# Performance work log

Hardware: AMD Instinct MI355X
Metric: run time of the kernel (lower is better)

## Reference

```python
import jax, jax.numpy as jnp
import numpy as np

COMMITMENT_COST = 0.25


def setup_inputs() -> dict:
    key = jax.random.key(0)
    k1, k2 = jax.random.split(key)
    # z_latents: [B, H, W, D] encoder output latents
    z_latents = jax.random.normal(k1, (128, 32, 32, 64), dtype=jnp.float32)
    # embeddings: [D, K] codebook, uniform init like tf.random_uniform_initializer (default [-0.05, 0.05])
    embeddings = jax.random.uniform(k2, (64, 1024), dtype=jnp.float32, minval=-0.05, maxval=0.05)
    return {"z_latents": z_latents, "embeddings": embeddings}


def reference(z_latents, embeddings):
    d, k = embeddings.shape
    flat = z_latents.reshape(-1, d)  # [N, D]
    # squared L2 distances to each codebook entry: [N, K]
    distances = (
        jnp.sum(flat * flat, axis=1, keepdims=True)
        - 2.0 * (flat @ embeddings)
        + jnp.sum(embeddings * embeddings, axis=0, keepdims=True)
    )
    # argmax(-d) == argmin(d) (both take first occurrence on ties)
    encoding_indices = jnp.argmin(distances, axis=1)  # [N]
    # one-hot @ embeddings.T is just a gather of codebook rows
    quantized = jnp.take(embeddings.T, encoding_indices, axis=0).reshape(z_latents.shape)
    commitment_loss = jnp.mean((jax.lax.stop_gradient(quantized) - z_latents) ** 2)
    embedding_loss = jnp.mean((jax.lax.stop_gradient(z_latents) - quantized) ** 2)
    vq_loss = embedding_loss + COMMITMENT_COST * commitment_loss
    # straight-through estimator
    quantized_st = z_latents + jax.lax.stop_gradient(quantized - z_latents)
    return quantized_st, vq_loss
```

## Files before the change

### kernel.cpp

```cpp
#include <hip/hip_runtime.h>

#pragma clang fp contract(off)

typedef __attribute__((ext_vector_type(8))) short short8;
typedef __attribute__((ext_vector_type(4))) float f32x4;

#define MARGIN 0.02f

static __device__ __forceinline__ unsigned short f2b(float f) {
    union { float f; unsigned u; } x; x.f = f;
    unsigned u = x.u;
    return (unsigned short)((u + 0x7FFFu + ((u >> 16) & 1u)) >> 16);
}

template <int ES>
static __device__ __forceinline__ float np_dist(
    const float* __restrict__ zr, const float* __restrict__ ecol,
    float zn, float en) {
    float c = 0.f;
    #pragma unroll
    for (int i = 0; i < 64; ++i) c = fmaf(zr[i], ecol[i * ES], c);
    float t = zn - 2.f * c;
    return t + en;
}

template <bool ET>
__global__ __launch_bounds__(256) void vq_prep(
    const float* __restrict__ E, float* __restrict__ enorm,
    float* __restrict__ Et, unsigned* __restrict__ EbW) {
    __shared__ float sT[64][65];
    const int tid = threadIdx.x;
    const int w = tid >> 6;
    const int m64 = tid & 63;
    const int c0 = blockIdx.x * 64;

    #pragma unroll
    for (int r = 0; r < 16; ++r) {
        const int row = r * 4 + w;
        sT[row][m64] = E[row * 1024 + c0 + m64];
    }
    __syncthreads();

    if (ET) {
        #pragma unroll
        for (int it = 0; it < 16; ++it) {
            const int e = it * 256 + tid;
            const int col = e >> 6, d = e & 63;
            Et[(c0 + col) * 64 + d] = sT[d][col];
        }
    }
    #pragma unroll
    for (int it = 0; it < 8; ++it) {
        const int w0 = it * 256 + tid;
        const int cl = w0 >> 9;
        const int s = (w0 >> 8) & 1;
        const int ll = (w0 >> 2) & 63;
        const int j = (w0 & 3) * 2;
        const int d = s * 32 + (ll >> 4) * 8 + j;
        const int col = cl * 16 + (ll & 15);
        const unsigned lo = f2b(sT[d][col]);
        const unsigned hi = f2b(sT[d + 1][col]);
        EbW[(blockIdx.x * 4 + cl) * 512 + (w0 & 511)] = lo | (hi << 16);
    }
    if (tid < 64) {
        float s2 = 0.f;
        #pragma unroll
        for (int d = 0; d < 64; ++d) {
            float v = sT[d][tid];
            s2 = fmaf(v, v, s2);
        }
        enorm[c0 + tid] = s2;
    }
}

template <int MODE>
__global__ __launch_bounds__(256, 8) void vq_main(
    const float* __restrict__ z, const float* __restrict__ E,
    const float* __restrict__ Et, const unsigned short* __restrict__ Eb,
    const float* __restrict__ enorm, float* __restrict__ out) {
    __shared__ unsigned short sB[2][4096];
    __shared__ float sEn[1024];

    float* sZn = (float*)&sB[0][0];
    int* sIdx = (int*)((char*)&sB[0][0] + 256);
    float* sRed = (float*)((char*)&sB[0][0] + 512);

    const int tid = threadIdx.x;
    const int w = tid >> 6;
    const int l = tid & 63;
    const int quad = l >> 4;
    const int m = l & 15;
    const int b = blockIdx.x;

    auto stage = [&](int h, int buf) {
        const unsigned short* gp = Eb + h * 4096 + w * 1024 + l * 8;
        unsigned short* lp = &sB[buf][w * 1024];
        #pragma unroll
        for (int i = 0; i < 2; ++i) {
            __builtin_amdgcn_global_load_lds(
                (const __attribute__((address_space(1))) void*)(gp + i * 512),
                (__attribute__((address_space(3))) void*)(lp + i * 512),
                16, 0, 0);
        }
    };

    if constexpr (MODE < 2) {
        stage(0, 0);
        stage(1, 1);
        float4 e4 = ((const float4*)enorm)[tid];
        e4.x *= 0.5f; e4.y *= 0.5f; e4.z *= 0.5f; e4.w *= 0.5f;
        ((float4*)sEn)[tid] = e4;
    } else {
        #pragma unroll
        for (int i = 0; i < 4; ++i) {
            const int col = tid + i * 256;
            float s2 = 0.f;
            #pragma unroll
            for (int d = 0; d < 64; ++d) {
                float v = E[d * 1024 + col];
                s2 = fmaf(v, v, s2);
            }
            sEn[col] = s2 * 0.5f;
        }
    }

    short8 a[2];
    {
        const int rowl = w * 16 + m;
        #pragma unroll
        for (int s = 0; s < 2; ++s) {
            const float* zp = z + (b * 64 + rowl) * 64 + s * 32 + quad * 8;
            union { float4 v; float f[4]; } u0, u1;
            u0.v = *(const float4*)zp;
            u1.v = *(const float4*)(zp + 4);
            short8 av;
            #pragma unroll
            for (int j = 0; j < 4; ++j) av[j] = (short)(f2b(u0.f[j]) ^ 0x8000u);
            #pragma unroll
            for (int j = 0; j < 4; ++j) av[4 + j] = (short)(f2b(u1.f[j]) ^ 0x8000u);
            a[s] = av;
        }
    }

    float v1p[4], v2p[4];
    #pragma unroll
    for (int r = 0; r < 4; ++r) { v1p[r] = 3.4e38f; v2p[r] = 3.4e38f; }

    if constexpr (MODE < 2) {
        asm volatile("s_waitcnt vmcnt(2) lgkmcnt(0)" ::: "memory");
        __builtin_amdgcn_sched_barrier(0);
        __builtin_amdgcn_s_barrier();

        for (int h = 0; h < 16; ++h) {
            const unsigned short* bufp = &sB[h & 1][l * 8];
            #pragma unroll
            for (int ct = 0; ct < 4; ++ct) {
                const int c = h * 4 + ct;
                short8 b0 = *(const short8*)(bufp + ct * 1024);
                short8 b1 = *(const short8*)(bufp + ct * 1024 + 512);
                const float enh = sEn[c * 16 + m];
                f32x4 acc = {enh, enh, enh, enh};
                acc = __builtin_amdgcn_mfma_f32_16x16x32_bf16(a[0], b0, acc, 0, 0, 0);
                acc = __builtin_amdgcn_mfma_f32_16x16x32_bf16(a[1], b1, acc, 0, 0, 0);
                #pragma unroll
                for (int r = 0; r < 4; ++r) {
                    float p0 = __uint_as_float(
                        (__float_as_uint(acc[r]) & 0xFFFFFFC0u) | (unsigned)c);
                    v2p[r] = __builtin_amdgcn_fmed3f(p0, v1p[r], v2p[r]);
                    v1p[r] = fminf(p0, v1p[r]);
                }
            }
            if (h == 15) break;
            __builtin_amdgcn_s_barrier();
            if (h < 14) {
                stage(h + 2, h & 1);
                asm volatile("s_waitcnt vmcnt(2)" ::: "memory");
            } else {
                asm volatile("s_waitcnt vmcnt(0)" ::: "memory");
            }
            __builtin_amdgcn_sched_barrier(0);
            __builtin_amdgcn_s_barrier();
        }
    } else {
        unsigned* sW = (unsigned*)&sB[0][0];
        __syncthreads();
        for (int h = 0; h < 16; ++h) {
            #pragma unroll
            for (int it = 0; it < 8; ++it) {
                const int w0 = it * 256 + tid;
                const int cl = w0 >> 9;
                const int s = (w0 >> 8) & 1;
                const int ll = (w0 >> 2) & 63;
                const int j = (w0 & 3) * 2;
                const int d = s * 32 + (ll >> 4) * 8 + j;
                const int col = (h * 4 + cl) * 16 + (ll & 15);
                const unsigned lo = f2b(E[d * 1024 + col]);
                const unsigned hi = f2b(E[(d + 1) * 1024 + col]);
                sW[w0] = lo | (hi << 16);
            }
            __syncthreads();
            const unsigned short* bufp = &sB[0][l * 8];
            #pragma unroll
            for (int ct = 0; ct < 4; ++ct) {
                const int c = h * 4 + ct;
                short8 b0 = *(const short8*)(bufp + ct * 1024);
                short8 b1 = *(const short8*)(bufp + ct * 1024 + 512);
                const float enh = sEn[c * 16 + m];
                f32x4 acc = {enh, enh, enh, enh};
                acc = __builtin_amdgcn_mfma_f32_16x16x32_bf16(a[0], b0, acc, 0, 0, 0);
                acc = __builtin_amdgcn_mfma_f32_16x16x32_bf16(a[1], b1, acc, 0, 0, 0);
                #pragma unroll
                for (int r = 0; r < 4; ++r) {
                    float p0 = __uint_as_float(
                        (__float_as_uint(acc[r]) & 0xFFFFFFC0u) | (unsigned)c);
                    v2p[r] = __builtin_amdgcn_fmed3f(p0, v1p[r], v2p[r]);
                    v1p[r] = fminf(p0, v1p[r]);
                }
            }
            __syncthreads();
        }
    }

    __syncthreads();

    if (l < 16) {
        const int row = w * 16 + l;
        const float* zr = z + (b * 64 + row) * 64;
        float S[16];
        #pragma unroll
        for (int u = 0; u < 16; ++u) { float v = zr[u]; S[u] = v * v; }
        #pragma unroll
        for (int t = 1; t < 4; ++t)
            #pragma unroll
            for (int u = 0; u < 16; ++u) {
                float v = zr[16 * t + u];
                float sq = v * v;
                S[u] = S[u] + sq;
            }
        float R0 = (S[0] + S[4]) + (S[8] + S[12]);
        float R1 = (S[1] + S[5]) + (S[9] + S[13]);
        float R2 = (S[2] + S[6]) + (S[10] + S[14]);
        float R3 = (S[3] + S[7]) + (S[11] + S[15]);
        sZn[row] = (R0 + R1) + (R2 + R3);
    }
    __syncthreads();

    constexpr bool viaEt = (MODE == 0);
    const float margin_q = MARGIN * 0.5f;
    float la = 0.f;
    #pragma unroll
    for (int r = 0; r < 4; ++r) {
        float pv1 = v1p[r];
        float vb = pv1;
        #pragma unroll
        for (int mask = 1; mask <= 8; mask <<= 1)
            vb = fminf(vb, __shfl_xor(vb, mask));
        const int rowl = w * 16 + quad * 4 + r;
        const float zn = sZn[rowl];
        const float* zr = z + (b * 64 + rowl) * 64;
        float d = 3.4e38f;
        int kk = 0x7fffffff;
        if (pv1 <= vb + margin_q) {
            kk = (int)(__float_as_uint(pv1) & 63u) * 16 + m;
            d = viaEt ? np_dist<1>(zr, Et + kk * 64, zn, 2.f * sEn[kk])
                      : np_dist<1024>(zr, E + kk, zn, 2.f * sEn[kk]);
        }
        float pv2 = v2p[r];
        if (pv2 <= vb + margin_q) {
            int kc = (int)(__float_as_uint(pv2) & 63u) * 16 + m;
            float dd = viaEt ? np_dist<1>(zr, Et + kc * 64, zn, 2.f * sEn[kc])
                             : np_dist<1024>(zr, E + kc, zn, 2.f * sEn[kc]);
            if (dd < d || (dd == d && kc < kk)) { d = dd; kk = kc; }
        }
        #pragma unroll
        for (int mask = 1; mask <= 8; mask <<= 1) {
            float d2 = __shfl_xor(d, mask);
            int c2 = __shfl_xor(kk, mask);
            bool take = (d2 < d) || (d2 == d && c2 < kk);
            d = take ? d2 : d;
            kk = take ? c2 : kk;
        }
        if (m == 0) {
            sIdx[rowl] = kk;
            la += d;
        }
    }
    __syncthreads();

    {
        const int row_local = w * 16 + (l >> 2);
        const int part = l & 3;
        const int idx = sIdx[row_local];
        union { float s[16]; float4 f[4]; } tmp;
        if (viaEt) {
            const float4* src = (const float4*)(Et + idx * 64 + part * 16);
            #pragma unroll
            for (int q4 = 0; q4 < 4; ++q4) tmp.f[q4] = src[q4];
        } else {
            #pragma unroll
            for (int dd = 0; dd < 16; ++dd) tmp.s[dd] = E[(part * 16 + dd) * 1024 + idx];
        }
        float4* dst = (float4*)(out + (b * 64 + row_local) * 64 + part * 16);
        #pragma unroll
        for (int q4 = 0; q4 < 4; ++q4) dst[q4] = tmp.f[q4];
    }

    #pragma unroll
    for (int mask = 32; mask >= 1; mask >>= 1) la += __shfl_xor(la, mask);
    if (l == 0) sRed[w] = la;
    __syncthreads();

    if (tid == 0) {
        const float blocksum = sRed[0] + sRed[1] + sRed[2] + sRed[3];
        atomicAdd(out + 8388608, blocksum * (1.25f / 8388608.f));
    }
}

extern "C" void kernel_launch(void* const* d_in, const int* in_sizes, int n_in,
                              void* d_out, int out_size, void* d_ws, size_t ws_size,
                              hipStream_t stream) {
    const float* z = (const float*)d_in[0];
    const float* E = (const float*)d_in[1];
    float* out = (float*)d_out;

    char* ws = (char*)d_ws;
    float* enorm = (float*)(ws + 128);
    unsigned short* Eb = (unsigned short*)(ws + 8192);
    float* Et = (float*)(ws + 139264);

    if (ws_size >= (size_t)401408) {
        vq_prep<true><<<16, 256, 0, stream>>>(E, enorm, Et, (unsigned*)Eb);
        vq_main<0><<<2048, 256, 0, stream>>>(z, E, Et, Eb, enorm, out);
    } else if (ws_size >= (size_t)139264) {
        vq_prep<false><<<16, 256, 0, stream>>>(E, enorm, Et, (unsigned*)Eb);
        vq_main<1><<<2048, 256, 0, stream>>>(z, E, Et, Eb, enorm, out);
    } else {
        vq_main<2><<<2048, 256, 0, stream>>>(z, E, Et, Eb, enorm, out);
    }
}
```

Baseline: 145.2 us.

## Use 512-thread blocks with 32 rows per wave and half-codebook LDS staging

Blocks now hold 8 waves, and each wave covers 32 rows as two 16-row MFMA tiles, so every B fragment read from LDS feeds two MFMA tiles. The bf16 codebook is staged in two halves of 64KB each rather than a double-buffered 4-chunk ring, which cuts the number of barriers from 30 to a few. Row norms are now computed before the main loop and shared with a shuffle instead of through LDS, and the indices are kept per wave, which removes several block syncs. The cost is much larger LDS per block (about 68KB), which lowers occupancy. Loads of the second half are also not overlapped with compute, so the wait is exposed.

```diff
diff --git a/kernel.cpp b/kernel.cpp
--- a/kernel.cpp
+++ b/kernel.cpp
@@ -74,16 +74,14 @@
 }
 
 template <int MODE>
-__global__ __launch_bounds__(256, 8) void vq_main(
+__global__ __launch_bounds__(512, 4) void vq_main(
     const float* __restrict__ z, const float* __restrict__ E,
     const float* __restrict__ Et, const unsigned short* __restrict__ Eb,
     const float* __restrict__ enorm, float* __restrict__ out) {
-    __shared__ unsigned short sB[2][4096];
+    __shared__ unsigned short sB[32768];
     __shared__ float sEn[1024];
-
-    float* sZn = (float*)&sB[0][0];
-    int* sIdx = (int*)((char*)&sB[0][0] + 256);
-    float* sRed = (float*)((char*)&sB[0][0] + 512);
+    __shared__ int sIdxW[8][32];
+    __shared__ float sRed[8];
 
     const int tid = threadIdx.x;
     const int w = tid >> 6;
@@ -91,12 +89,13 @@
     const int quad = l >> 4;
     const int m = l & 15;
     const int b = blockIdx.x;
-
-    auto stage = [&](int h, int buf) {
-        const unsigned short* gp = Eb + h * 4096 + w * 1024 + l * 8;
-        unsigned short* lp = &sB[buf][w * 1024];
-        #pragma unroll
-        for (int i = 0; i < 2; ++i) {
+    const int R0 = (b * 8 + w) * 32;
+
+    auto stageH = [&](int H) {
+        const unsigned short* gp = Eb + H * 32768 + w * 4096 + l * 8;
+        unsigned short* lp = &sB[w * 4096];
+        #pragma unroll
+        for (int i = 0; i < 8; ++i) {
             __builtin_amdgcn_global_load_lds(
                 (const __attribute__((address_space(1))) void*)(gp + i * 512),
                 (__attribute__((address_space(3))) void*)(lp + i * 512),
@@ -104,16 +103,32 @@
         }
     };
 
+    auto convertH = [&](int H) {
+        unsigned* sW = (unsigned*)&sB[0];
+        #pragma unroll
+        for (int it = 0; it < 32; ++it) {
+            const int W = it * 512 + tid;
+            const int cl = W >> 9;
+            const int s2 = (W >> 8) & 1;
+            const int ll = (W >> 2) & 63;
+            const int j = (W & 3) * 2;
+            const int d = s2 * 32 + (ll >> 4) * 8 + j;
+            const int col = (H * 32 + cl) * 16 + (ll & 15);
+            const unsigned lo = f2b(E[d * 1024 + col]);
+            const unsigned hi = f2b(E[(d + 1) * 1024 + col]);
+            sW[W] = lo | (hi << 16);
+        }
+    };
+
     if constexpr (MODE < 2) {
-        stage(0, 0);
-        stage(1, 1);
-        float4 e4 = ((const float4*)enorm)[tid];
-        e4.x *= 0.5f; e4.y *= 0.5f; e4.z *= 0.5f; e4.w *= 0.5f;
-        ((float4*)sEn)[tid] = e4;
+        stageH(0);
+        float2 e2 = ((const float2*)enorm)[tid];
+        e2.x *= 0.5f; e2.y *= 0.5f;
+        ((float2*)sEn)[tid] = e2;
     } else {
         #pragma unroll
-        for (int i = 0; i < 4; ++i) {
-            const int col = tid + i * 256;
+        for (int i = 0; i < 2; ++i) {
+            const int col = tid + i * 512;
             float s2 = 0.f;
             #pragma unroll
             for (int d = 0; d < 64; ++d) {
@@ -122,14 +137,15 @@
             }
             sEn[col] = s2 * 0.5f;
         }
-    }
-
-    short8 a[2];
-    {
-        const int rowl = w * 16 + m;
-        #pragma unroll
-        for (int s = 0; s < 2; ++s) {
-            const float* zp = z + (b * 64 + rowl) * 64 + s * 32 + quad * 8;
+        convertH(0);
+    }
+
+    short8 a0[2], a1[2];
+    #pragma unroll
+    for (int s = 0; s < 2; ++s) {
+        #pragma unroll
+        for (int s2 = 0; s2 < 2; ++s2) {
+            const float* zp = z + (R0 + s * 16 + m) * 64 + s2 * 32 + quad * 8;
             union { float4 v; float f[4]; } u0, u1;
             u0.v = *(const float4*)zp;
             u1.v = *(const float4*)(zp + 4);
@@ -138,169 +154,139 @@
             for (int j = 0; j < 4; ++j) av[j] = (short)(f2b(u0.f[j]) ^ 0x8000u);
             #pragma unroll
             for (int j = 0; j < 4; ++j) av[4 + j] = (short)(f2b(u1.f[j]) ^ 0x8000u);
-            a[s] = av;
-        }
-    }
-
-    float v1p[4], v2p[4];
-    #pragma unroll
-    for (int r = 0; r < 4; ++r) { v1p[r] = 3.4e38f; v2p[r] = 3.4e38f; }
-
-    if constexpr (MODE < 2) {
-        asm volatile("s_waitcnt vmcnt(2) lgkmcnt(0)" ::: "memory");
+            if (s == 0) a0[s2] = av; else a1[s2] = av;
+        }
+    }
+
+    float zn0 = 0.f, zn1 = 0.f;
+    #pragma unroll
+    for (int s = 0; s < 2; ++s) {
+        if (l < 16) {
+            const float* zr = z + (R0 + s * 16 + l) * 64;
+            float S[16];
+            #pragma unroll
+            for (int u = 0; u < 16; ++u) { float v = zr[u]; S[u] = v * v; }
+            #pragma unroll
+            for (int t = 1; t < 4; ++t)
+                #pragma unroll
+                for (int u = 0; u < 16; ++u) {
+                    float v = zr[16 * t + u];
+                    float sq = v * v;
+                    S[u] = S[u] + sq;
+                }
+            float Ra = (S[0] + S[4]) + (S[8] + S[12]);
+            float Rb = (S[1] + S[5]) + (S[9] + S[13]);
+            float Rc = (S[2] + S[6]) + (S[10] + S[14]);
+            float Rd = (S[3] + S[7]) + (S[11] + S[15]);
+            float zn = (Ra + Rb) + (Rc + Rd);
+            if (s == 0) zn0 = zn; else zn1 = zn;
+        }
+    }
+
+    float v1p[2][4], v2p[2][4];
+    #pragma unroll
+    for (int s = 0; s < 2; ++s)
+        #pragma unroll
+        for (int r = 0; r < 4; ++r) { v1p[s][r] = 3.4e38f; v2p[s][r] = 3.4e38f; }
+
+    #pragma unroll
+    for (int H = 0; H < 2; ++H) {
+        if (H == 1) {
+            __syncthreads();
+            if constexpr (MODE < 2) stageH(1); else convertH(1);
+        }
+        asm volatile("s_waitcnt vmcnt(0) lgkmcnt(0)" ::: "memory");
         __builtin_amdgcn_sched_barrier(0);
         __builtin_amdgcn_s_barrier();
 
-        for (int h = 0; h < 16; ++h) {
-            const unsigned short* bufp = &sB[h & 1][l * 8];
-            #pragma unroll
-            for (int ct = 0; ct < 4; ++ct) {
-                const int c = h * 4 + ct;
-                short8 b0 = *(const short8*)(bufp + ct * 1024);
-                short8 b1 = *(const short8*)(bufp + ct * 1024 + 512);
-                const float enh = sEn[c * 16 + m];
-                f32x4 acc = {enh, enh, enh, enh};
-                acc = __builtin_amdgcn_mfma_f32_16x16x32_bf16(a[0], b0, acc, 0, 0, 0);
-                acc = __builtin_amdgcn_mfma_f32_16x16x32_bf16(a[1], b1, acc, 0, 0, 0);
-                #pragma unroll
-                for (int r = 0; r < 4; ++r) {
-                    float p0 = __uint_as_float(
-                        (__float_as_uint(acc[r]) & 0xFFFFFFC0u) | (unsigned)c);
-                    v2p[r] = __builtin_amdgcn_fmed3f(p0, v1p[r], v2p[r]);
-                    v1p[r] = fminf(p0, v1p[r]);
-                }
-            }
-            if (h == 15) break;
-            __builtin_amdgcn_s_barrier();
-            if (h < 14) {
-                stage(h + 2, h & 1);
-                asm volatile("s_waitcnt vmcnt(2)" ::: "memory");
-            } else {
-                asm volatile("s_waitcnt vmcnt(0)" ::: "memory");
-            }
-            __builtin_amdgcn_sched_barrier(0);
-            __builtin_amdgcn_s_barrier();
-        }
-    } else {
-        unsigned* sW = (unsigned*)&sB[0][0];
-        __syncthreads();
-        for (int h = 0; h < 16; ++h) {
-            #pragma unroll
-            for (int it = 0; it < 8; ++it) {
-                const int w0 = it * 256 + tid;
-                const int cl = w0 >> 9;
-                const int s = (w0 >> 8) & 1;
-                const int ll = (w0 >> 2) & 63;
-                const int j = (w0 & 3) * 2;
-                const int d = s * 32 + (ll >> 4) * 8 + j;
-                const int col = (h * 4 + cl) * 16 + (ll & 15);
-                const unsigned lo = f2b(E[d * 1024 + col]);
-                const unsigned hi = f2b(E[(d + 1) * 1024 + col]);
-                sW[w0] = lo | (hi << 16);
-            }
-            __syncthreads();
-            const unsigned short* bufp = &sB[0][l * 8];
-            #pragma unroll
-            for (int ct = 0; ct < 4; ++ct) {
-                const int c = h * 4 + ct;
-                short8 b0 = *(const short8*)(bufp + ct * 1024);
-                short8 b1 = *(const short8*)(bufp + ct * 1024 + 512);
-                const float enh = sEn[c * 16 + m];
-                f32x4 acc = {enh, enh, enh, enh};
-                acc = __builtin_amdgcn_mfma_f32_16x16x32_bf16(a[0], b0, acc, 0, 0, 0);
-                acc = __builtin_amdgcn_mfma_f32_16x16x32_bf16(a[1], b1, acc, 0, 0, 0);
-                #pragma unroll
-                for (int r = 0; r < 4; ++r) {
-                    float p0 = __uint_as_float(
-                        (__float_as_uint(acc[r]) & 0xFFFFFFC0u) | (unsigned)c);
-                    v2p[r] = __builtin_amdgcn_fmed3f(p0, v1p[r], v2p[r]);
-                    v1p[r] = fminf(p0, v1p[r]);
-                }
-            }
-            __syncthreads();
-        }
-    }
-
-    __syncthreads();
-
-    if (l < 16) {
-        const int row = w * 16 + l;
-        const float* zr = z + (b * 64 + row) * 64;
-        float S[16];
-        #pragma unroll
-        for (int u = 0; u < 16; ++u) { float v = zr[u]; S[u] = v * v; }
-        #pragma unroll
-        for (int t = 1; t < 4; ++t)
-            #pragma unroll
-            for (int u = 0; u < 16; ++u) {
-                float v = zr[16 * t + u];
-                float sq = v * v;
-                S[u] = S[u] + sq;
-            }
-        float R0 = (S[0] + S[4]) + (S[8] + S[12]);
-        float R1 = (S[1] + S[5]) + (S[9] + S[13]);
-        float R2 = (S[2] + S[6]) + (S[10] + S[14]);
-        float R3 = (S[3] + S[7]) + (S[11] + S[15]);
-        sZn[row] = (R0 + R1) + (R2 + R3);
-    }
-    __syncthreads();
+        #pragma unroll 4
+        for (int c = 0; c < 32; ++c) {
+            const int gc = H * 32 + c;
+            short8 b0 = *(const short8*)&sB[c * 1024 + l * 8];
+            short8 b1 = *(const short8*)&sB[c * 1024 + 512 + l * 8];
+            const float enh = sEn[gc * 16 + m];
+            f32x4 acc0 = {enh, enh, enh, enh};
+            f32x4 acc1 = {enh, enh, enh, enh};
+            acc0 = __builtin_amdgcn_mfma_f32_16x16x32_bf16(a0[0], b0, acc0, 0, 0, 0);
+            acc0 = __builtin_amdgcn_mfma_f32_16x16x32_bf16(a0[1], b1, acc0, 0, 0, 0);
+            acc1 = __builtin_amdgcn_mfma_f32_16x16x32_bf16(a1[0], b0, acc1, 0, 0, 0);
+            acc1 = __builtin_amdgcn_mfma_f32_16x16x32_bf16(a1[1], b1, acc1, 0, 0, 0);
+            #pragma unroll
+            for (int r = 0; r < 4; ++r) {
+                float p0 = __uint_as_float(
+                    (__float_as_uint(acc0[r]) & 0xFFFFFFC0u) | (unsigned)gc);
+                v2p[0][r] = __builtin_amdgcn_fmed3f(p0, v1p[0][r], v2p[0][r]);
+                v1p[0][r] = fminf(p0, v1p[0][r]);
+                float p1 = __uint_as_float(
+                    (__float_as_uint(acc1[r]) & 0xFFFFFFC0u) | (unsigned)gc);
+                v2p[1][r] = __builtin_amdgcn_fmed3f(p1, v1p[1][r], v2p[1][r]);
+                v1p[1][r] = fminf(p1, v1p[1][r]);
+            }
+        }
+    }
 
     constexpr bool viaEt = (MODE == 0);
     const float margin_q = MARGIN * 0.5f;
     float la = 0.f;
     #pragma unroll
-    for (int r = 0; r < 4; ++r) {
-        float pv1 = v1p[r];
-        float vb = pv1;
-        #pragma unroll
-        for (int mask = 1; mask <= 8; mask <<= 1)
-            vb = fminf(vb, __shfl_xor(vb, mask));
-        const int rowl = w * 16 + quad * 4 + r;
-        const float zn = sZn[rowl];
-        const float* zr = z + (b * 64 + rowl) * 64;
-        float d = 3.4e38f;
-        int kk = 0x7fffffff;
-        if (pv1 <= vb + margin_q) {
-            kk = (int)(__float_as_uint(pv1) & 63u) * 16 + m;
-            d = viaEt ? np_dist<1>(zr, Et + kk * 64, zn, 2.f * sEn[kk])
-                      : np_dist<1024>(zr, E + kk, zn, 2.f * sEn[kk]);
-        }
-        float pv2 = v2p[r];
-        if (pv2 <= vb + margin_q) {
-            int kc = (int)(__float_as_uint(pv2) & 63u) * 16 + m;
-            float dd = viaEt ? np_dist<1>(zr, Et + kc * 64, zn, 2.f * sEn[kc])
-                             : np_dist<1024>(zr, E + kc, zn, 2.f * sEn[kc]);
-            if (dd < d || (dd == d && kc < kk)) { d = dd; kk = kc; }
-        }
-        #pragma unroll
-        for (int mask = 1; mask <= 8; mask <<= 1) {
-            float d2 = __shfl_xor(d, mask);
-            int c2 = __shfl_xor(kk, mask);
-            bool take = (d2 < d) || (d2 == d && c2 < kk);
-            d = take ? d2 : d;
-            kk = take ? c2 : kk;
-        }
-        if (m == 0) {
-            sIdx[rowl] = kk;
-            la += d;
-        }
-    }
-    __syncthreads();
-
-    {
-        const int row_local = w * 16 + (l >> 2);
+    for (int s = 0; s < 2; ++s) {
+        #pragma unroll
+        for (int r = 0; r < 4; ++r) {
+            float pv1 = v1p[s][r];
+            float vb = pv1;
+            #pragma unroll
+            for (int mask = 1; mask <= 8; mask <<= 1)
+                vb = fminf(vb, __shfl_xor(vb, mask));
+            const int rowls = quad * 4 + r;
+            const float zn = __shfl(s == 0 ? zn0 : zn1, rowls);
+            const float* zr = z + (R0 + s * 16 + rowls) * 64;
+            float d = 3.4e38f;
+            int kk = 0x7fffffff;
+            if (pv1 <= vb + margin_q) {
+                kk = (int)(__float_as_uint(pv1) & 63u) * 16 + m;
+                d = viaEt ? np_dist<1>(zr, Et + kk * 64, zn, 2.f * sEn[kk])
+                          : np_dist<1024>(zr, E + kk, zn, 2.f * sEn[kk]);
+            }
+            float pv2 = v2p[s][r];
+            if (pv2 <= vb + margin_q) {
+                int kc = (int)(__float_as_uint(pv2) & 63u) * 16 + m;
+                float dd = viaEt ? np_dist<1>(zr, Et + kc * 64, zn, 2.f * sEn[kc])
+                                 : np_dist<1024>(zr, E + kc, zn, 2.f * sEn[kc]);
+                if (dd < d || (dd == d && kc < kk)) { d = dd; kk = kc; }
+            }
+            #pragma unroll
+            for (int mask = 1; mask <= 8; mask <<= 1) {
+                float d2 = __shfl_xor(d, mask);
+                int c2 = __shfl_xor(kk, mask);
+                bool take = (d2 < d) || (d2 == d && c2 < kk);
+                d = take ? d2 : d;
+                kk = take ? c2 : kk;
+            }
+            if (m == 0) {
+                sIdxW[w][s * 16 + rowls] = kk;
+                la += d;
+            }
+        }
+    }
+
+    asm volatile("s_waitcnt lgkmcnt(0)" ::: "memory");
+
+    #pragma unroll
+    for (int s = 0; s < 2; ++s) {
+        const int row_in = l >> 2;
         const int part = l & 3;
-        const int idx = sIdx[row_local];
-        union { float s[16]; float4 f[4]; } tmp;
+        const int idx = sIdxW[w][s * 16 + row_in];
+        union { float ss[16]; float4 f[4]; } tmp;
         if (viaEt) {
             const float4* src = (const float4*)(Et + idx * 64 + part * 16);
             #pragma unroll
             for (int q4 = 0; q4 < 4; ++q4) tmp.f[q4] = src[q4];
         } else {
             #pragma unroll
-            for (int dd = 0; dd < 16; ++dd) tmp.s[dd] = E[(part * 16 + dd) * 1024 + idx];
-        }
-        float4* dst = (float4*)(out + (b * 64 + row_local) * 64 + part * 16);
+            for (int dd = 0; dd < 16; ++dd)
+                tmp.ss[dd] = E[(part * 16 + dd) * 1024 + idx];
+        }
+        float4* dst = (float4*)(out + (R0 + s * 16 + row_in) * 64 + part * 16);
         #pragma unroll
         for (int q4 = 0; q4 < 4; ++q4) dst[q4] = tmp.f[q4];
     }
@@ -309,10 +295,11 @@
     for (int mask = 32; mask >= 1; mask >>= 1) la += __shfl_xor(la, mask);
     if (l == 0) sRed[w] = la;
     __syncthreads();
-
     if (tid == 0) {
-        const float blocksum = sRed[0] + sRed[1] + sRed[2] + sRed[3];
-        atomicAdd(out + 8388608, blocksum * (1.25f / 8388608.f));
+        float bs = 0.f;
+        #pragma unroll
+        for (int i = 0; i < 8; ++i) bs += sRed[i];
+        atomicAdd(out + 8388608, bs * (1.25f / 8388608.f));
     }
 }
 
@@ -330,11 +317,11 @@
 
     if (ws_size >= (size_t)401408) {
         vq_prep<true><<<16, 256, 0, stream>>>(E, enorm, Et, (unsigned*)Eb);
-        vq_main<0><<<2048, 256, 0, stream>>>(z, E, Et, Eb, enorm, out);
+        vq_main<0><<<512, 512, 0, stream>>>(z, E, Et, Eb, enorm, out);
     } else if (ws_size >= (size_t)139264) {
         vq_prep<false><<<16, 256, 0, stream>>>(E, enorm, Et, (unsigned*)Eb);
-        vq_main<1><<<2048, 256, 0, stream>>>(z, E, Et, Eb, enorm, out);
+        vq_main<1><<<512, 512, 0, stream>>>(z, E, Et, Eb, enorm, out);
     } else {
-        vq_main<2><<<2048, 256, 0, stream>>>(z, E, Et, Eb, enorm, out);
-    }
-}
+        vq_main<2><<<512, 512, 0, stream>>>(z, E, Et, Eb, enorm, out);
+    }
+}
```

Measured after the change: 143.1 us. No clear change (-1.5%).
